# Optimization experiments

Measured on AMD Instinct MI355X. Metric: run time of the kernel, lower is better.

Reference implementation:

```python
import jax, jax.numpy as jnp
import numpy as np


def setup_inputs() -> dict:
    key = jax.random.key(0)
    ks = jax.random.split(key, 5)
    t, b, s, d = 4, 4, 1024, 512
    x = jax.random.normal(ks[0], (t, b, s, d), dtype=jnp.float32)
    wq = jax.random.normal(ks[1], (d, d), dtype=jnp.float32) * 0.02
    wk = jax.random.normal(ks[2], (d, d), dtype=jnp.float32) * 0.02
    wv = jax.random.normal(ks[3], (d, d), dtype=jnp.float32) * 0.02
    wo = jax.random.normal(ks[4], (d, d), dtype=jnp.float32) * 0.02
    z = jnp.zeros((d,), dtype=jnp.float32)
    return {"x": x, "wq": wq, "bq": z, "wk": wk, "bk": z, "wv": wv,
            "bv": z, "wo": wo, "bo": z, "num_heads": 8}


def reference(x, wq, bq, wk, bk, wv, bv, wo, bo, num_heads):
    t, b, s, d = x.shape
    dh = d // num_heads
    # QKV projections (torch Linear stores weight as [out,in]; here weights are
    # random square matrices so x @ w + b is the same math)
    q = x @ wq + bq
    k = x @ wk + bk
    v = x @ wv + bv
    # Faithful to source: plain row-major view to (t*b*h, s, dh) WITHOUT
    # transposing a head axis (this mixes seq blocks into the batch-of-heads dim)
    q = q.reshape(t * b * num_heads, s, dh)
    k = k.reshape(t * b * num_heads, s, dh)
    v = v.reshape(t * b * num_heads, s, dh)
    scale = 1.0 / jnp.sqrt(jnp.float32(dh))
    scores = jnp.einsum('bqd,bkd->bqk', q, k) * scale  # [t*b*h, s, s]
    attn = jax.nn.softmax(scores, axis=-1)
    out = jnp.einsum('bqk,bkd->bqd', attn, v)  # [t*b*h, s, dh]
    out = out.reshape(t, b, s, d)
    return out @ wo + bo
```

## Files before the change

kernel.cpp:

```cpp
#include <hip/hip_runtime.h>

typedef __bf16 bf16;
typedef __bf16 bf16x4 __attribute__((ext_vector_type(4)));
typedef __bf16 bf16x8 __attribute__((ext_vector_type(8)));
typedef float  f32x4  __attribute__((ext_vector_type(4)));
typedef float  f32x16 __attribute__((ext_vector_type(16)));
typedef unsigned int u32x4 __attribute__((ext_vector_type(4)));

#define MFMA16(a, b, c) __builtin_amdgcn_mfma_f32_16x16x32_bf16((a), (b), (c), 0, 0, 0)
#define MFMA32(a, b, c) __builtin_amdgcn_mfma_f32_32x32x16_bf16((a), (b), (c), 0, 0, 0)
#define SW(row, g) (((row) << 6) + ((((g) ^ ((row) & 7))) << 3))

#define QSCALE 0.1803368801111137f

typedef __attribute__((address_space(3))) uint32_t       lds_u32_t;
typedef const __attribute__((address_space(1))) uint32_t glob_u32_t;

__device__ __forceinline__ void ld_lds16(const bf16* g, bf16* l) {
    __builtin_amdgcn_global_load_lds((glob_u32_t*)g, (lds_u32_t*)l, 16, 0, 0);
}

__global__ __launch_bounds__(256) void prep(
    const float* __restrict__ X,
    const float* __restrict__ wq, const float* __restrict__ wk,
    const float* __restrict__ wv, const float* __restrict__ wo,
    bf16* __restrict__ Xb, bf16* __restrict__ wqkvT, bf16* __restrict__ woT)
{
    int bid = blockIdx.x;
    if (bid < 4096) {
        size_t i = ((size_t)bid * 256 + threadIdx.x) * 8;
        const f32x4* s = (const f32x4*)(X + i);
        f32x4 a = s[0], b = s[1];
        bf16x8 o;
        for (int e = 0; e < 4; e++) { o[e] = (bf16)a[e]; o[e + 4] = (bf16)b[e]; }
        *(bf16x8*)(Xb + i) = o;
    } else {
        int idx = (bid - 4096) * 256 + threadIdx.x;
        int which = idx >> 15;
        int r = idx & 32767;
        int kg = r >> 9, n = r & 511;
        const float* w = (which == 0) ? wq : (which == 1) ? wk : (which == 2) ? wv : wo;
        bf16x8 o;
        for (int e = 0; e < 8; e++) o[e] = (bf16)w[(size_t)(kg * 8 + e) * 512 + n];
        bf16* dst = ((which < 3) ? (wqkvT + (size_t)which * 262144) : woT) + (size_t)n * 512 + kg * 8;
        *(bf16x8*)dst = o;
    }
}

__global__ __launch_bounds__(256, 4) void gemm_qkv(
    const bf16* __restrict__ Xb, const bf16* __restrict__ WT,
    const float* __restrict__ bq, const float* __restrict__ bk,
    const float* __restrict__ bv,
    bf16* __restrict__ Q, bf16* __restrict__ K, bf16* __restrict__ V)
{
    __shared__ char smem[34816];
    bf16* As = (bf16*)smem;
    bf16* Bs = (bf16*)(smem + 16384);

    const int t = threadIdx.x;
    const int lane = t & 63, wid = t >> 6;
    const int wr = wid >> 1, wc = wid & 1;
    const int lr = lane & 15, quad = lane >> 4;
    const int bid = blockIdx.x;
    const int xcd = bid & 7, j0 = bid >> 3;
    const int m0 = (xcd * 16 + (j0 & 15)) * 128;
    const int x = j0 >> 4;
    const int which = x >> 2;
    const int n0 = (x & 3) * 128;
    const bf16* Wt = WT + (size_t)which * 262144;

    f32x4 zf = {0.f, 0.f, 0.f, 0.f};
    f32x4 acc[4][4];
    for (int i = 0; i < 4; i++)
        for (int jj = 0; jj < 4; jj++) acc[i][jj] = zf;

    const int srow = t >> 3;
    const int sg = (t & 7) ^ (srow & 7);
    const bf16* gA = Xb + (size_t)(m0 + srow) * 512 + sg * 8;
    const bf16* gB = Wt + (size_t)(n0 + srow) * 512 + sg * 8;
    bf16* lA = As + t * 8;
    bf16* lB = Bs + t * 8;

    for (int k0 = 0; k0 < 512; k0 += 64) {
        for (int p = 0; p < 4; p++) {
            ld_lds16(gA + k0 + p * 32 * 512, lA + p * 2048);
            ld_lds16(gB + k0 + p * 32 * 512, lB + p * 2048);
        }
        __syncthreads();
        for (int kk = 0; kk < 2; ++kk) {
            bf16x8 af[4], bf_[4];
            for (int i = 0; i < 4; i++)
                af[i] = *(const bf16x8*)&As[SW(wr * 64 + i * 16 + lr, kk * 4 + quad)];
            for (int jj = 0; jj < 4; jj++)
                bf_[jj] = *(const bf16x8*)&Bs[SW(wc * 64 + jj * 16 + lr, kk * 4 + quad)];
            for (int i = 0; i < 4; i++)
                for (int jj = 0; jj < 4; jj++)
                    acc[i][jj] = MFMA16(af[i], bf_[jj], acc[i][jj]);
        }
        __syncthreads();
    }

    bf16* OUT = (which == 0) ? Q : (which == 1) ? K : V;
    const float* bias = (which == 0) ? bq : (which == 1) ? bk : bv;
    const float qs = (which == 0) ? QSCALE : 1.0f;

    bf16* Ep = (bf16*)smem + wid * 4352;
    for (int jj = 0; jj < 4; jj++) {
        int n = n0 + wc * 64 + jj * 16 + lr;
        float bb = bias[n];
        for (int i = 0; i < 4; i++) {
            int row = i * 16 + quad * 4;
            for (int r = 0; r < 4; r++)
                Ep[(row + r) * 68 + jj * 16 + lr] = (bf16)((acc[i][jj][r] + bb) * qs);
        }
    }
    bf16* wO = OUT + (size_t)(m0 + wr * 64) * 512 + n0 + wc * 64;
    for (int s = 0; s < 8; s++) {
        int row = s * 8 + (lane >> 3), g = lane & 7;
        *(bf16x8*)(wO + (size_t)row * 512 + g * 8) = *(const bf16x8*)&Ep[row * 68 + g * 8];
    }
}

__global__ __launch_bounds__(256, 4) void gemm_out(
    const bf16* __restrict__ A, const bf16* __restrict__ WoT,
    const float* __restrict__ bo, float* __restrict__ OUT)
{
    __shared__ char smem[34816];
    bf16* As = (bf16*)smem;
    bf16* Bs = (bf16*)(smem + 16384);

    const int t = threadIdx.x;
    const int lane = t & 63, wid = t >> 6;
    const int wr = wid >> 1, wc = wid & 1;
    const int lr = lane & 15, quad = lane >> 4;
    const int bid = blockIdx.x;
    const int xcd = bid & 7, j0 = bid >> 3;
    const int m0 = (xcd * 16 + (j0 & 15)) * 128;
    const int n0 = (j0 >> 4) * 128;

    f32x4 zf = {0.f, 0.f, 0.f, 0.f};
    f32x4 acc[4][4];
    for (int i = 0; i < 4; i++)
        for (int jj = 0; jj < 4; jj++) acc[i][jj] = zf;

    const int srow = t >> 3;
    const int sg = (t & 7) ^ (srow & 7);
    const bf16* gA = A + (size_t)(m0 + srow) * 512 + sg * 8;
    const bf16* gB = WoT + (size_t)(n0 + srow) * 512 + sg * 8;
    bf16* lA = As + t * 8;
    bf16* lB = Bs + t * 8;

    for (int k0 = 0; k0 < 512; k0 += 64) {
        for (int p = 0; p < 4; p++) {
            ld_lds16(gA + k0 + p * 32 * 512, lA + p * 2048);
            ld_lds16(gB + k0 + p * 32 * 512, lB + p * 2048);
        }
        __syncthreads();
        for (int kk = 0; kk < 2; ++kk) {
            bf16x8 af[4], bf_[4];
            for (int i = 0; i < 4; i++)
                af[i] = *(const bf16x8*)&As[SW(wr * 64 + i * 16 + lr, kk * 4 + quad)];
            for (int jj = 0; jj < 4; jj++)
                bf_[jj] = *(const bf16x8*)&Bs[SW(wc * 64 + jj * 16 + lr, kk * 4 + quad)];
            for (int i = 0; i < 4; i++)
                for (int jj = 0; jj < 4; jj++)
                    acc[i][jj] = MFMA16(af[i], bf_[jj], acc[i][jj]);
        }
        __syncthreads();
    }

    float bb[4];
    for (int jj = 0; jj < 4; jj++) bb[jj] = bo[n0 + wc * 64 + jj * 16 + lr];

    float* Ef = (float*)smem + wid * 2112;
    for (int h = 0; h < 2; h++) {
        for (int jj = 0; jj < 4; jj++)
            for (int ii = 0; ii < 2; ii++) {
                int i = h * 2 + ii;
                int row = ii * 16 + quad * 4;
                for (int r = 0; r < 4; r++)
                    Ef[(row + r) * 66 + jj * 16 + lr] = acc[i][jj][r] + bb[jj];
            }
        float* wO = OUT + (size_t)(m0 + wr * 64 + h * 32) * 512 + n0 + wc * 64;
        for (int s = 0; s < 8; s++) {
            int row = s * 4 + (lane >> 4), c = (lane & 15) * 4;
            *(f32x4*)(wO + (size_t)row * 512 + c) = *(const f32x4*)&Ef[row * 66 + c];
        }
        __syncthreads();
    }
}

__global__ __launch_bounds__(256) void transpose_v(
    const bf16* __restrict__ V, bf16* __restrict__ VT)
{
    __shared__ bf16 L[64 * 72];
    const int t = threadIdx.x;
    const int b = blockIdx.y, kb = blockIdx.x;
    const bf16* src = V + ((size_t)b * 1024 + (size_t)kb * 64) * 64;
    const int row = t >> 2, c0 = (t & 3) * 16;
    *(bf16x8*)&L[row * 72 + c0]     = *(const bf16x8*)(src + row * 64 + c0);
    *(bf16x8*)&L[row * 72 + c0 + 8] = *(const bf16x8*)(src + row * 64 + c0 + 8);
    __syncthreads();
    bf16x8 o0, o1;
    for (int e = 0; e < 8; e++) {
        o0[e] = L[(c0 + e) * 72 + row];
        o1[e] = L[(c0 + 8 + e) * 72 + row];
    }
    bf16* dst = VT + ((size_t)b * 64 + row) * 1024 + (size_t)kb * 64 + c0;
    *(bf16x8*)dst       = o0;
    *(bf16x8*)(dst + 8) = o1;
}

__global__ __launch_bounds__(256, 4) void attn(
    const bf16* __restrict__ Q, const bf16* __restrict__ K,
    const bf16* __restrict__ VT, bf16* __restrict__ O)
{
    __shared__ char smem[32768];
    bf16* const K0 = (bf16*)smem;
    bf16* const V0 = (bf16*)(smem + 8192);
    bf16* const K1 = (bf16*)(smem + 16384);
    bf16* const V1 = (bf16*)(smem + 24576);

    const int t = threadIdx.x, lane = t & 63, wid = t >> 6;
    const int q31 = lane & 31, hi = lane >> 5;
    const int bid = blockIdx.x;
    const int batch = (bid & 7) * 16 + ((bid >> 3) & 15);
    const int q0 = (bid >> 7) * 128;
    const bf16* Qb = Q + (size_t)batch * 65536;
    const bf16* Kb = K + (size_t)batch * 65536;
    const bf16* Vb = VT + (size_t)batch * 65536;

    bf16x8 qf[4];
#pragma unroll
    for (int kk = 0; kk < 4; ++kk)
        qf[kk] = *(const bf16x8*)(Qb + (size_t)(q0 + wid * 32 + q31) * 64 + kk * 16 + hi * 8);

    f32x16 oacc[2];
#pragma unroll
    for (int ct = 0; ct < 2; ++ct)
#pragma unroll
        for (int r = 0; r < 16; ++r) oacc[ct][r] = 0.f;
    float lsum = 0.f;

    const int srow = t >> 3;
    const int sg8 = ((t & 7) ^ (srow & 7)) * 8;

#define STAGE(ktile, KD, VD) do {                                        \
        const bf16* gK_ = Kb + (size_t)(ktile) * 4096;                   \
        const bf16* gV_ = Vb + (size_t)(ktile) * 64;                     \
        ld_lds16(gK_ + srow * 64 + sg8,                  (KD) + t * 8);  \
        ld_lds16(gK_ + (srow + 32) * 64 + sg8,           (KD) + t * 8 + 2048); \
        ld_lds16(gV_ + (size_t)srow * 1024 + sg8,        (VD) + t * 8);  \
        ld_lds16(gV_ + (size_t)(srow + 32) * 1024 + sg8, (VD) + t * 8 + 2048); \
    } while (0)

    STAGE(0, K0, V0);

    for (int kt = 0; kt < 16; ++kt) {
        bf16* Kt = (kt & 1) ? K1 : K0;
        bf16* Vt = (kt & 1) ? V1 : V0;
        bf16* Kn = (kt & 1) ? K0 : K1;
        bf16* Vn = (kt & 1) ? V0 : V1;

        __builtin_amdgcn_sched_barrier(0);
        __builtin_amdgcn_s_barrier();
        __builtin_amdgcn_sched_barrier(0);
        if (kt < 15) {
            STAGE(kt + 1, Kn, Vn);
            asm volatile("s_waitcnt vmcnt(4)" ::: "memory");
        } else {
            asm volatile("s_waitcnt vmcnt(0)" ::: "memory");
        }
        __builtin_amdgcn_sched_barrier(0);
        __builtin_amdgcn_s_barrier();
        __builtin_amdgcn_sched_barrier(0);

        f32x16 sacc[2];
#pragma unroll
        for (int i2 = 0; i2 < 2; ++i2)
#pragma unroll
            for (int r = 0; r < 16; ++r) sacc[i2][r] = 0.f;

        __builtin_amdgcn_s_setprio(1);
#pragma unroll
        for (int kk = 0; kk < 4; ++kk) {
            bf16x8 a0 = *(const bf16x8*)&Kt[SW(q31, kk * 2 + hi)];
            bf16x8 a1 = *(const bf16x8*)&Kt[SW(32 + q31, kk * 2 + hi)];
            sacc[0] = MFMA32(a0, qf[kk], sacc[0]);
            sacc[1] = MFMA32(a1, qf[kk], sacc[1]);
        }
        __builtin_amdgcn_s_setprio(0);

        float ls = 0.f;
#pragma unroll
        for (int i2 = 0; i2 < 2; ++i2)
#pragma unroll
            for (int r = 0; r < 16; ++r) {
                float p = __builtin_amdgcn_exp2f(sacc[i2][r]);
                ls += p;
                sacc[i2][r] = p;
            }
        lsum += ls;

        bf16x8 pa[4];
#pragma unroll
        for (int c = 0; c < 4; ++c) {
            const int i2 = c >> 1, rb = (c & 1) * 8;
            uint32_t x0, x1, x2, x3;
            asm("v_cvt_pk_bf16_f32 %0, %1, %2" : "=v"(x0) : "v"(sacc[i2][rb + 0]), "v"(sacc[i2][rb + 1]));
            asm("v_cvt_pk_bf16_f32 %0, %1, %2" : "=v"(x1) : "v"(sacc[i2][rb + 2]), "v"(sacc[i2][rb + 3]));
            asm("v_cvt_pk_bf16_f32 %0, %1, %2" : "=v"(x2) : "v"(sacc[i2][rb + 4]), "v"(sacc[i2][rb + 5]));
            asm("v_cvt_pk_bf16_f32 %0, %1, %2" : "=v"(x3) : "v"(sacc[i2][rb + 6]), "v"(sacc[i2][rb + 7]));
            asm volatile("v_permlane32_swap_b32 %0, %1" : "+v"(x0), "+v"(x2));
            asm volatile("v_permlane32_swap_b32 %0, %1" : "+v"(x1), "+v"(x3));
            u32x4 w = {x0, x1, x2, x3};
            pa[c] = __builtin_bit_cast(bf16x8, w);
        }

        __builtin_amdgcn_s_setprio(1);
#pragma unroll
        for (int c = 0; c < 4; ++c)
#pragma unroll
            for (int ct = 0; ct < 2; ++ct) {
                bf16x8 bv = *(const bf16x8*)&Vt[SW(ct * 32 + q31, c * 2 + hi)];
                oacc[ct] = MFMA32(pa[c], bv, oacc[ct]);
            }
        __builtin_amdgcn_s_setprio(0);
    }
#undef STAGE

    lsum += __shfl_xor(lsum, 32, 64);
    const float invl = 1.f / lsum;

    __syncthreads();
    bf16* Ep = (bf16*)smem + wid * 2176;
#pragma unroll
    for (int r = 0; r < 16; ++r) {
        const int ql = (r & 3) + 8 * (r >> 2) + 4 * hi;
        const float im = __shfl(invl, ql, 64);
        Ep[ql * 68 + q31]      = (bf16)(oacc[0][r] * im);
        Ep[ql * 68 + 32 + q31] = (bf16)(oacc[1][r] * im);
    }
    bf16* Ob = O + (size_t)batch * 65536 + (size_t)(q0 + wid * 32) * 64;
#pragma unroll
    for (int s = 0; s < 4; s++) {
        int row = s * 8 + (lane >> 3), g = lane & 7;
        *(bf16x8*)(Ob + (size_t)row * 64 + g * 8) = *(const bf16x8*)&Ep[row * 68 + g * 8];
    }
}

extern "C" void kernel_launch(void* const* d_in, const int* in_sizes, int n_in,
                              void* d_out, int out_size, void* d_ws, size_t ws_size,
                              hipStream_t stream)
{
    const float* x  = (const float*)d_in[0];
    const float* wq = (const float*)d_in[1];
    const float* bq = (const float*)d_in[2];
    const float* wk = (const float*)d_in[3];
    const float* bk = (const float*)d_in[4];
    const float* wv = (const float*)d_in[5];
    const float* bv = (const float*)d_in[6];
    const float* wo = (const float*)d_in[7];
    const float* bo = (const float*)d_in[8];

    char* ws = (char*)d_ws;
    bf16* wqkvT = (bf16*)ws;
    bf16* woT   = (bf16*)(ws + 1572864);
    bf16* Xb    = (bf16*)(ws + 2097152);
    bf16* VTb   = Xb;
    bf16* Qb    = (bf16*)(ws + 2097152 + 16777216ull);
    bf16* Kb    = (bf16*)(ws + 2097152 + 2 * 16777216ull);
    bf16* Vb    = (bf16*)(ws + 2097152 + 3 * 16777216ull);
    bf16* Ab    = Vb;

    prep<<<4608, 256, 0, stream>>>(x, wq, wk, wv, wo, Xb, wqkvT, woT);
    gemm_qkv<<<1536, 256, 0, stream>>>(Xb, wqkvT, bq, bk, bv, Qb, Kb, Vb);
    transpose_v<<<dim3(16, 128), 256, 0, stream>>>(Vb, VTb);
    attn<<<1024, 256, 0, stream>>>(Qb, Kb, VTb, Ab);
    gemm_out<<<512, 256, 0, stream>>>(Ab, woT, bo, (float*)d_out);
}
```

Measured before the change: 202.5 us.

## Process two 32-query tiles per wave in attention to reuse K/V fragments

Each wave in the attention kernel now owns 64 query rows (two 32-row MFMA tiles) instead of 32, so each block covers 256 queries and the grid halves to 512 blocks. Every K and V fragment read from LDS now feeds two MFMAs instead of one. This halves LDS read traffic and global K/V staging per unit of work. The cost is doubled accumulator and score registers per thread, so launch bounds drop to 2 blocks per CU, which lowers occupancy and weakens latency hiding.

Result: faster. 197.6 us (-2.4%).

```diff
diff --git a/kernel.cpp b/kernel.cpp
--- a/kernel.cpp
+++ b/kernel.cpp
@@ -211,7 +211,7 @@
     *(bf16x8*)(dst + 8) = o1;
 }
 
-__global__ __launch_bounds__(256, 4) void attn(
+__global__ __launch_bounds__(256, 2) void attn(
     const bf16* __restrict__ Q, const bf16* __restrict__ K,
     const bf16* __restrict__ VT, bf16* __restrict__ O)
 {
@@ -225,22 +225,26 @@
     const int q31 = lane & 31, hi = lane >> 5;
     const int bid = blockIdx.x;
     const int batch = (bid & 7) * 16 + ((bid >> 3) & 15);
-    const int q0 = (bid >> 7) * 128;
+    const int q0 = (bid >> 7) * 256;
     const bf16* Qb = Q + (size_t)batch * 65536;
     const bf16* Kb = K + (size_t)batch * 65536;
     const bf16* Vb = VT + (size_t)batch * 65536;
 
-    bf16x8 qf[4];
-#pragma unroll
-    for (int kk = 0; kk < 4; ++kk)
-        qf[kk] = *(const bf16x8*)(Qb + (size_t)(q0 + wid * 32 + q31) * 64 + kk * 16 + hi * 8);
-
-    f32x16 oacc[2];
-#pragma unroll
-    for (int ct = 0; ct < 2; ++ct)
-#pragma unroll
-        for (int r = 0; r < 16; ++r) oacc[ct][r] = 0.f;
-    float lsum = 0.f;
+    bf16x8 qf[2][4];
+#pragma unroll
+    for (int jq = 0; jq < 2; ++jq)
+#pragma unroll
+        for (int kk = 0; kk < 4; ++kk)
+            qf[jq][kk] = *(const bf16x8*)(Qb + (size_t)(q0 + wid * 64 + jq * 32 + q31) * 64 + kk * 16 + hi * 8);
+
+    f32x16 oacc[2][2];
+#pragma unroll
+    for (int jq = 0; jq < 2; ++jq)
+#pragma unroll
+        for (int ct = 0; ct < 2; ++ct)
+#pragma unroll
+            for (int r = 0; r < 16; ++r) oacc[jq][ct][r] = 0.f;
+    float lsum[2] = {0.f, 0.f};
 
     const int srow = t >> 3;
     const int sg8 = ((t & 7) ^ (srow & 7)) * 8;
@@ -275,46 +279,53 @@
         __builtin_amdgcn_s_barrier();
         __builtin_amdgcn_sched_barrier(0);
 
-        f32x16 sacc[2];
-#pragma unroll
-        for (int i2 = 0; i2 < 2; ++i2)
-#pragma unroll
-            for (int r = 0; r < 16; ++r) sacc[i2][r] = 0.f;
+        f32x16 sacc[2][2];
+#pragma unroll
+        for (int jq = 0; jq < 2; ++jq)
+#pragma unroll
+            for (int i2 = 0; i2 < 2; ++i2)
+#pragma unroll
+                for (int r = 0; r < 16; ++r) sacc[jq][i2][r] = 0.f;
 
         __builtin_amdgcn_s_setprio(1);
 #pragma unroll
         for (int kk = 0; kk < 4; ++kk) {
             bf16x8 a0 = *(const bf16x8*)&Kt[SW(q31, kk * 2 + hi)];
             bf16x8 a1 = *(const bf16x8*)&Kt[SW(32 + q31, kk * 2 + hi)];
-            sacc[0] = MFMA32(a0, qf[kk], sacc[0]);
-            sacc[1] = MFMA32(a1, qf[kk], sacc[1]);
+            sacc[0][0] = MFMA32(a0, qf[0][kk], sacc[0][0]);
+            sacc[1][0] = MFMA32(a0, qf[1][kk], sacc[1][0]);
+            sacc[0][1] = MFMA32(a1, qf[0][kk], sacc[0][1]);
+            sacc[1][1] = MFMA32(a1, qf[1][kk], sacc[1][1]);
         }
         __builtin_amdgcn_s_setprio(0);
 
-        float ls = 0.f;
-#pragma unroll
-        for (int i2 = 0; i2 < 2; ++i2)
-#pragma unroll
-            for (int r = 0; r < 16; ++r) {
-                float p = __builtin_amdgcn_exp2f(sacc[i2][r]);
-                ls += p;
-                sacc[i2][r] = p;
+        bf16x8 pa[2][4];
+#pragma unroll
+        for (int jq = 0; jq < 2; ++jq) {
+            float ls = 0.f;
+#pragma unroll
+            for (int i2 = 0; i2 < 2; ++i2)
+#pragma unroll
+                for (int r = 0; r < 16; ++r) {
+                    float p = __builtin_amdgcn_exp2f(sacc[jq][i2][r]);
+                    ls += p;
+                    sacc[jq][i2][r] = p;
+                }
+            lsum[jq] += ls;
+
+#pragma unroll
+            for (int c = 0; c < 4; ++c) {
+                const int i2 = c >> 1, rb = (c & 1) * 8;
+                uint32_t x0, x1, x2, x3;
+                asm("v_cvt_pk_bf16_f32 %0, %1, %2" : "=v"(x0) : "v"(sacc[jq][i2][rb + 0]), "v"(sacc[jq][i2][rb + 1]));
+                asm("v_cvt_pk_bf16_f32 %0, %1, %2" : "=v"(x1) : "v"(sacc[jq][i2][rb + 2]), "v"(sacc[jq][i2][rb + 3]));
+                asm("v_cvt_pk_bf16_f32 %0, %1, %2" : "=v"(x2) : "v"(sacc[jq][i2][rb + 4]), "v"(sacc[jq][i2][rb + 5]));
+                asm("v_cvt_pk_bf16_f32 %0, %1, %2" : "=v"(x3) : "v"(sacc[jq][i2][rb + 6]), "v"(sacc[jq][i2][rb + 7]));
+                asm volatile("v_permlane32_swap_b32 %0, %1" : "+v"(x0), "+v"(x2));
+                asm volatile("v_permlane32_swap_b32 %0, %1" : "+v"(x1), "+v"(x3));
+                u32x4 w = {x0, x1, x2, x3};
+                pa[jq][c] = __builtin_bit_cast(bf16x8, w);
             }
-        lsum += ls;
-
-        bf16x8 pa[4];
-#pragma unroll
-        for (int c = 0; c < 4; ++c) {
-            const int i2 = c >> 1, rb = (c & 1) * 8;
-            uint32_t x0, x1, x2, x3;
-            asm("v_cvt_pk_bf16_f32 %0, %1, %2" : "=v"(x0) : "v"(sacc[i2][rb + 0]), "v"(sacc[i2][rb + 1]));
-            asm("v_cvt_pk_bf16_f32 %0, %1, %2" : "=v"(x1) : "v"(sacc[i2][rb + 2]), "v"(sacc[i2][rb + 3]));
-            asm("v_cvt_pk_bf16_f32 %0, %1, %2" : "=v"(x2) : "v"(sacc[i2][rb + 4]), "v"(sacc[i2][rb + 5]));
-            asm("v_cvt_pk_bf16_f32 %0, %1, %2" : "=v"(x3) : "v"(sacc[i2][rb + 6]), "v"(sacc[i2][rb + 7]));
-            asm volatile("v_permlane32_swap_b32 %0, %1" : "+v"(x0), "+v"(x2));
-            asm volatile("v_permlane32_swap_b32 %0, %1" : "+v"(x1), "+v"(x3));
-            u32x4 w = {x0, x1, x2, x3};
-            pa[c] = __builtin_bit_cast(bf16x8, w);
         }
 
         __builtin_amdgcn_s_setprio(1);
@@ -323,29 +334,37 @@
 #pragma unroll
             for (int ct = 0; ct < 2; ++ct) {
                 bf16x8 bv = *(const bf16x8*)&Vt[SW(ct * 32 + q31, c * 2 + hi)];
-                oacc[ct] = MFMA32(pa[c], bv, oacc[ct]);
+                oacc[0][ct] = MFMA32(pa[0][c], bv, oacc[0][ct]);
+                oacc[1][ct] = MFMA32(pa[1][c], bv, oacc[1][ct]);
             }
         __builtin_amdgcn_s_setprio(0);
     }
 #undef STAGE
 
-    lsum += __shfl_xor(lsum, 32, 64);
-    const float invl = 1.f / lsum;
+    float invl[2];
+#pragma unroll
+    for (int jq = 0; jq < 2; ++jq) {
+        lsum[jq] += __shfl_xor(lsum[jq], 32, 64);
+        invl[jq] = 1.f / lsum[jq];
+    }
 
     __syncthreads();
     bf16* Ep = (bf16*)smem + wid * 2176;
 #pragma unroll
-    for (int r = 0; r < 16; ++r) {
-        const int ql = (r & 3) + 8 * (r >> 2) + 4 * hi;
-        const float im = __shfl(invl, ql, 64);
-        Ep[ql * 68 + q31]      = (bf16)(oacc[0][r] * im);
-        Ep[ql * 68 + 32 + q31] = (bf16)(oacc[1][r] * im);
-    }
-    bf16* Ob = O + (size_t)batch * 65536 + (size_t)(q0 + wid * 32) * 64;
-#pragma unroll
-    for (int s = 0; s < 4; s++) {
-        int row = s * 8 + (lane >> 3), g = lane & 7;
-        *(bf16x8*)(Ob + (size_t)row * 64 + g * 8) = *(const bf16x8*)&Ep[row * 68 + g * 8];
+    for (int jq = 0; jq < 2; ++jq) {
+#pragma unroll
+        for (int r = 0; r < 16; ++r) {
+            const int ql = (r & 3) + 8 * (r >> 2) + 4 * hi;
+            const float im = __shfl(invl[jq], ql, 64);
+            Ep[ql * 68 + q31]      = (bf16)(oacc[jq][0][r] * im);
+            Ep[ql * 68 + 32 + q31] = (bf16)(oacc[jq][1][r] * im);
+        }
+        bf16* Ob = O + (size_t)batch * 65536 + (size_t)(q0 + wid * 64 + jq * 32) * 64;
+#pragma unroll
+        for (int s = 0; s < 4; s++) {
+            int row = s * 8 + (lane >> 3), g = lane & 7;
+            *(bf16x8*)(Ob + (size_t)row * 64 + g * 8) = *(const bf16x8*)&Ep[row * 68 + g * 8];
+        }
     }
 }
 
@@ -376,6 +395,6 @@
     prep<<<4608, 256, 0, stream>>>(x, wq, wk, wv, wo, Xb, wqkvT, woT);
     gemm_qkv<<<1536, 256, 0, stream>>>(Xb, wqkvT, bq, bk, bv, Qb, Kb, Vb);
     transpose_v<<<dim3(16, 128), 256, 0, stream>>>(Vb, VTb);
-    attn<<<1024, 256, 0, stream>>>(Qb, Kb, VTb, Ab);
+    attn<<<512, 256, 0, stream>>>(Qb, Kb, VTb, Ab);
     gemm_out<<<512, 256, 0, stream>>>(Ab, woT, bo, (float*)d_out);
 }
```

## Interleave exp/convert with PV MFMAs and stagger block start with s_sleep

Applied to the files above, without the earlier changes.

Moves the softmax exp, row-sum and bf16 packing into the per-chunk loop so each chunk's PV MFMAs can overlap the exp work of the next chunk. The first QK MFMA now takes a hoisted zero accumulator instead of zeroing per iteration, and setprio stays high for the whole compute phase. The permlane asm statements lose their volatile qualifier so the compiler may reorder them. It also adds a small s_sleep stagger keyed on block index to spread out memory bursts, which adds idle time at block start.

After: 198.0 us. 2.2% less time.

```diff
diff --git a/kernel.cpp b/kernel.cpp
--- a/kernel.cpp
+++ b/kernel.cpp
@@ -230,10 +230,21 @@
     const bf16* Kb = K + (size_t)batch * 65536;
     const bf16* Vb = VT + (size_t)batch * 65536;
 
+    switch ((bid >> 8) & 3) {
+        case 1: __builtin_amdgcn_s_sleep(16); break;
+        case 2: __builtin_amdgcn_s_sleep(32); break;
+        case 3: __builtin_amdgcn_s_sleep(48); break;
+        default: break;
+    }
+
     bf16x8 qf[4];
 #pragma unroll
     for (int kk = 0; kk < 4; ++kk)
         qf[kk] = *(const bf16x8*)(Qb + (size_t)(q0 + wid * 32 + q31) * 64 + kk * 16 + hi * 8);
+
+    f32x16 kZero;
+#pragma unroll
+    for (int r = 0; r < 16; ++r) kZero[r] = 0.f;
 
     f32x16 oacc[2];
 #pragma unroll
@@ -275,56 +286,49 @@
         __builtin_amdgcn_s_barrier();
         __builtin_amdgcn_sched_barrier(0);
 
+        __builtin_amdgcn_s_setprio(1);
+
         f32x16 sacc[2];
-#pragma unroll
-        for (int i2 = 0; i2 < 2; ++i2)
-#pragma unroll
-            for (int r = 0; r < 16; ++r) sacc[i2][r] = 0.f;
-
-        __builtin_amdgcn_s_setprio(1);
-#pragma unroll
-        for (int kk = 0; kk < 4; ++kk) {
+        {
+            bf16x8 a0 = *(const bf16x8*)&Kt[SW(q31, hi)];
+            bf16x8 a1 = *(const bf16x8*)&Kt[SW(32 + q31, hi)];
+            sacc[0] = MFMA32(a0, qf[0], kZero);
+            sacc[1] = MFMA32(a1, qf[0], kZero);
+        }
+#pragma unroll
+        for (int kk = 1; kk < 4; ++kk) {
             bf16x8 a0 = *(const bf16x8*)&Kt[SW(q31, kk * 2 + hi)];
             bf16x8 a1 = *(const bf16x8*)&Kt[SW(32 + q31, kk * 2 + hi)];
             sacc[0] = MFMA32(a0, qf[kk], sacc[0]);
             sacc[1] = MFMA32(a1, qf[kk], sacc[1]);
         }
-        __builtin_amdgcn_s_setprio(0);
-
-        float ls = 0.f;
-#pragma unroll
-        for (int i2 = 0; i2 < 2; ++i2)
-#pragma unroll
-            for (int r = 0; r < 16; ++r) {
-                float p = __builtin_amdgcn_exp2f(sacc[i2][r]);
-                ls += p;
-                sacc[i2][r] = p;
-            }
-        lsum += ls;
-
-        bf16x8 pa[4];
+
 #pragma unroll
         for (int c = 0; c < 4; ++c) {
             const int i2 = c >> 1, rb = (c & 1) * 8;
+            float ls = 0.f;
+#pragma unroll
+            for (int e = 0; e < 8; ++e) {
+                float p = __builtin_amdgcn_exp2f(sacc[i2][rb + e]);
+                ls += p;
+                sacc[i2][rb + e] = p;
+            }
+            lsum += ls;
             uint32_t x0, x1, x2, x3;
             asm("v_cvt_pk_bf16_f32 %0, %1, %2" : "=v"(x0) : "v"(sacc[i2][rb + 0]), "v"(sacc[i2][rb + 1]));
             asm("v_cvt_pk_bf16_f32 %0, %1, %2" : "=v"(x1) : "v"(sacc[i2][rb + 2]), "v"(sacc[i2][rb + 3]));
             asm("v_cvt_pk_bf16_f32 %0, %1, %2" : "=v"(x2) : "v"(sacc[i2][rb + 4]), "v"(sacc[i2][rb + 5]));
             asm("v_cvt_pk_bf16_f32 %0, %1, %2" : "=v"(x3) : "v"(sacc[i2][rb + 6]), "v"(sacc[i2][rb + 7]));
-            asm volatile("v_permlane32_swap_b32 %0, %1" : "+v"(x0), "+v"(x2));
-            asm volatile("v_permlane32_swap_b32 %0, %1" : "+v"(x1), "+v"(x3));
+            asm("v_permlane32_swap_b32 %0, %1" : "+v"(x0), "+v"(x2));
+            asm("v_permlane32_swap_b32 %0, %1" : "+v"(x1), "+v"(x3));
             u32x4 w = {x0, x1, x2, x3};
-            pa[c] = __builtin_bit_cast(bf16x8, w);
-        }
-
-        __builtin_amdgcn_s_setprio(1);
-#pragma unroll
-        for (int c = 0; c < 4; ++c)
+            bf16x8 pa = __builtin_bit_cast(bf16x8, w);
 #pragma unroll
             for (int ct = 0; ct < 2; ++ct) {
                 bf16x8 bv = *(const bf16x8*)&Vt[SW(ct * 32 + q31, c * 2 + hi)];
-                oacc[ct] = MFMA32(pa[c], bv, oacc[ct]);
+                oacc[ct] = MFMA32(pa, bv, oacc[ct]);
             }
+        }
         __builtin_amdgcn_s_setprio(0);
     }
 #undef STAGE
```

## Software-pipeline QK and softmax-PV halves across key tiles with triple-buffered V

Applied to the files above, without the earlier changes.

Splits each 64-key tile into two 32-key halves. The second half's softmax and PV multiply is deferred into the next iteration, interleaved between QK MFMAs. V gets a third LDS buffer so the deferred half can still read the previous tile's V while the next one is staged. The aim is to overlap exp/convert VALU work with MFMA work; the cost is more LDS (40KB), which may reduce occupancy, and a fully unrolled loop.

Measured after the change: 493.5 us. 144% more time.

```diff
diff --git a/kernel.cpp b/kernel.cpp
--- a/kernel.cpp
+++ b/kernel.cpp
@@ -215,11 +215,10 @@
     const bf16* __restrict__ Q, const bf16* __restrict__ K,
     const bf16* __restrict__ VT, bf16* __restrict__ O)
 {
-    __shared__ char smem[32768];
-    bf16* const K0 = (bf16*)smem;
-    bf16* const V0 = (bf16*)(smem + 8192);
-    bf16* const K1 = (bf16*)(smem + 16384);
-    bf16* const V1 = (bf16*)(smem + 24576);
+    __shared__ char smem[40960];
+    bf16* const KL[2] = {(bf16*)smem, (bf16*)(smem + 8192)};
+    bf16* const VL[3] = {(bf16*)(smem + 16384), (bf16*)(smem + 24576),
+                         (bf16*)(smem + 32768)};
 
     const int t = threadIdx.x, lane = t & 63, wid = t >> 6;
     const int q31 = lane & 31, hi = lane >> 5;
@@ -245,28 +244,72 @@
     const int srow = t >> 3;
     const int sg8 = ((t & 7) ^ (srow & 7)) * 8;
 
-#define STAGE(ktile, KD, VD) do {                                        \
+#define STAGE_K(ktile, KD) do {                                          \
         const bf16* gK_ = Kb + (size_t)(ktile) * 4096;                   \
+        ld_lds16(gK_ + srow * 64 + sg8,        (KD) + t * 8);            \
+        ld_lds16(gK_ + (srow + 32) * 64 + sg8, (KD) + t * 8 + 2048);     \
+    } while (0)
+#define STAGE_V(ktile, VD) do {                                          \
         const bf16* gV_ = Vb + (size_t)(ktile) * 64;                     \
-        ld_lds16(gK_ + srow * 64 + sg8,                  (KD) + t * 8);  \
-        ld_lds16(gK_ + (srow + 32) * 64 + sg8,           (KD) + t * 8 + 2048); \
         ld_lds16(gV_ + (size_t)srow * 1024 + sg8,        (VD) + t * 8);  \
         ld_lds16(gV_ + (size_t)(srow + 32) * 1024 + sg8, (VD) + t * 8 + 2048); \
     } while (0)
 
-    STAGE(0, K0, V0);
-
+#define QK_HALF(KT, H, S) do {                                               \
+    _Pragma("unroll")                                                        \
+    for (int r_ = 0; r_ < 16; ++r_) S[r_] = 0.f;                             \
+    __builtin_amdgcn_s_setprio(1);                                           \
+    _Pragma("unroll")                                                        \
+    for (int kk_ = 0; kk_ < 4; ++kk_) {                                      \
+        bf16x8 a_ = *(const bf16x8*)&(KT)[SW((H) * 32 + q31, kk_ * 2 + hi)]; \
+        S = MFMA32(a_, qf[kk_], S);                                          \
+    }                                                                        \
+    __builtin_amdgcn_s_setprio(0);                                           \
+} while (0)
+
+#define SMPV_HALF(S, VTP, CBASE) do {                                        \
+    _Pragma("unroll")                                                        \
+    for (int c_ = 0; c_ < 2; ++c_) {                                         \
+        const int rb_ = c_ * 8, cc_ = (CBASE) + c_;                          \
+        float ls_ = 0.f;                                                     \
+        _Pragma("unroll")                                                    \
+        for (int e_ = 0; e_ < 8; ++e_) {                                     \
+            float p_ = __builtin_amdgcn_exp2f(S[rb_ + e_]);                  \
+            ls_ += p_;                                                       \
+            S[rb_ + e_] = p_;                                                \
+        }                                                                    \
+        lsum += ls_;                                                         \
+        uint32_t x0_, x1_, x2_, x3_;                                         \
+        asm("v_cvt_pk_bf16_f32 %0, %1, %2" : "=v"(x0_) : "v"(S[rb_ + 0]), "v"(S[rb_ + 1])); \
+        asm("v_cvt_pk_bf16_f32 %0, %1, %2" : "=v"(x1_) : "v"(S[rb_ + 2]), "v"(S[rb_ + 3])); \
+        asm("v_cvt_pk_bf16_f32 %0, %1, %2" : "=v"(x2_) : "v"(S[rb_ + 4]), "v"(S[rb_ + 5])); \
+        asm("v_cvt_pk_bf16_f32 %0, %1, %2" : "=v"(x3_) : "v"(S[rb_ + 6]), "v"(S[rb_ + 7])); \
+        asm("v_permlane32_swap_b32 %0, %1" : "+v"(x0_), "+v"(x2_));          \
+        asm("v_permlane32_swap_b32 %0, %1" : "+v"(x1_), "+v"(x3_));          \
+        u32x4 w_ = {x0_, x1_, x2_, x3_};                                     \
+        bf16x8 pa_ = __builtin_bit_cast(bf16x8, w_);                         \
+        __builtin_amdgcn_s_setprio(1);                                       \
+        bf16x8 bv0_ = *(const bf16x8*)&(VTP)[SW(q31, cc_ * 2 + hi)];         \
+        bf16x8 bv1_ = *(const bf16x8*)&(VTP)[SW(32 + q31, cc_ * 2 + hi)];    \
+        oacc[0] = MFMA32(pa_, bv0_, oacc[0]);                                \
+        oacc[1] = MFMA32(pa_, bv1_, oacc[1]);                                \
+        __builtin_amdgcn_s_setprio(0);                                       \
+    }                                                                        \
+} while (0)
+
+    STAGE_K(0, KL[0]);
+    STAGE_V(0, VL[0]);
+
+    f32x16 sA, sB;
+
+#pragma unroll
     for (int kt = 0; kt < 16; ++kt) {
-        bf16* Kt = (kt & 1) ? K1 : K0;
-        bf16* Vt = (kt & 1) ? V1 : V0;
-        bf16* Kn = (kt & 1) ? K0 : K1;
-        bf16* Vn = (kt & 1) ? V0 : V1;
-
         __builtin_amdgcn_sched_barrier(0);
         __builtin_amdgcn_s_barrier();
         __builtin_amdgcn_sched_barrier(0);
         if (kt < 15) {
-            STAGE(kt + 1, Kn, Vn);
+            STAGE_K(kt + 1, KL[(kt + 1) & 1]);
+            STAGE_V(kt + 1, VL[(kt + 1) % 3]);
             asm volatile("s_waitcnt vmcnt(4)" ::: "memory");
         } else {
             asm volatile("s_waitcnt vmcnt(0)" ::: "memory");
@@ -275,59 +318,19 @@
         __builtin_amdgcn_s_barrier();
         __builtin_amdgcn_sched_barrier(0);
 
-        f32x16 sacc[2];
-#pragma unroll
-        for (int i2 = 0; i2 < 2; ++i2)
-#pragma unroll
-            for (int r = 0; r < 16; ++r) sacc[i2][r] = 0.f;
-
-        __builtin_amdgcn_s_setprio(1);
-#pragma unroll
-        for (int kk = 0; kk < 4; ++kk) {
-            bf16x8 a0 = *(const bf16x8*)&Kt[SW(q31, kk * 2 + hi)];
-            bf16x8 a1 = *(const bf16x8*)&Kt[SW(32 + q31, kk * 2 + hi)];
-            sacc[0] = MFMA32(a0, qf[kk], sacc[0]);
-            sacc[1] = MFMA32(a1, qf[kk], sacc[1]);
-        }
-        __builtin_amdgcn_s_setprio(0);
-
-        float ls = 0.f;
-#pragma unroll
-        for (int i2 = 0; i2 < 2; ++i2)
-#pragma unroll
-            for (int r = 0; r < 16; ++r) {
-                float p = __builtin_amdgcn_exp2f(sacc[i2][r]);
-                ls += p;
-                sacc[i2][r] = p;
-            }
-        lsum += ls;
-
-        bf16x8 pa[4];
-#pragma unroll
-        for (int c = 0; c < 4; ++c) {
-            const int i2 = c >> 1, rb = (c & 1) * 8;
-            uint32_t x0, x1, x2, x3;
-            asm("v_cvt_pk_bf16_f32 %0, %1, %2" : "=v"(x0) : "v"(sacc[i2][rb + 0]), "v"(sacc[i2][rb + 1]));
-            asm("v_cvt_pk_bf16_f32 %0, %1, %2" : "=v"(x1) : "v"(sacc[i2][rb + 2]), "v"(sacc[i2][rb + 3]));
-            asm("v_cvt_pk_bf16_f32 %0, %1, %2" : "=v"(x2) : "v"(sacc[i2][rb + 4]), "v"(sacc[i2][rb + 5]));
-            asm("v_cvt_pk_bf16_f32 %0, %1, %2" : "=v"(x3) : "v"(sacc[i2][rb + 6]), "v"(sacc[i2][rb + 7]));
-            asm volatile("v_permlane32_swap_b32 %0, %1" : "+v"(x0), "+v"(x2));
-            asm volatile("v_permlane32_swap_b32 %0, %1" : "+v"(x1), "+v"(x3));
-            u32x4 w = {x0, x1, x2, x3};
-            pa[c] = __builtin_bit_cast(bf16x8, w);
-        }
-
-        __builtin_amdgcn_s_setprio(1);
-#pragma unroll
-        for (int c = 0; c < 4; ++c)
-#pragma unroll
-            for (int ct = 0; ct < 2; ++ct) {
-                bf16x8 bv = *(const bf16x8*)&Vt[SW(ct * 32 + q31, c * 2 + hi)];
-                oacc[ct] = MFMA32(pa[c], bv, oacc[ct]);
-            }
-        __builtin_amdgcn_s_setprio(0);
-    }
-#undef STAGE
+        const bf16* Kt = KL[kt & 1];
+        QK_HALF(Kt, 0, sA);
+        if (kt > 0)
+            SMPV_HALF(sB, VL[(kt + 2) % 3], 2);
+        QK_HALF(Kt, 1, sB);
+        SMPV_HALF(sA, VL[kt % 3], 0);
+    }
+    SMPV_HALF(sB, VL[0], 2);
+
+#undef STAGE_K
+#undef STAGE_V
+#undef QK_HALF
+#undef SMPV_HALF
 
     lsum += __shfl_xor(lsum, 32, 64);
     const float invl = 1.f / lsum;
```
